# Kernel optimization log

Measured on AMD Instinct MI355X. Metric: run time of the kernel, lower is better.

## Reference

```python
import jax, jax.numpy as jnp
import numpy as np

SHIFT = 3
SHIFT2 = 1
POOL_K = 9
MAX_LEN = 16384
BATCH = 256


def _avg_pool1d(x, k, s):
    # x: [..., L] -> VALID average pool over last axis
    acc = jax.lax.reduce_window(x, 0.0, jax.lax.add,
                                (1,) * (x.ndim - 1) + (k,),
                                (1,) * (x.ndim - 1) + (s,), 'VALID')
    return acc / k


def _max_pool1d(x, k, s):
    return jax.lax.reduce_window(x, -jnp.inf, jax.lax.max,
                                 (1,) * (x.ndim - 1) + (k,),
                                 (1,) * (x.ndim - 1) + (s,), 'VALID')


def _upsample_nearest(x, size):
    # torch nn.Upsample(mode='nearest') to target length `size`
    m = x.shape[-1]
    idx = (jnp.arange(size) * m) // size
    return x[..., idx]


def setup_inputs() -> dict:
    key = jax.random.key(0)
    x = jax.random.normal(key, (BATCH, MAX_LEN), dtype=jnp.float32)
    return {"x": x}


def reference(x) -> jnp.ndarray:
    # First derivatives: fixed conv [[-1],[1]] over (rolled, original) row pairs
    # is exactly diff_d = x - roll(x, 2^d).  [B, shift, L]
    deriv1 = jnp.stack([x - jnp.roll(x, 1 << d, axis=-1) for d in range(SHIFT)], axis=1)
    # Second derivatives from the first diff channel (deriv1[:, 0]).
    d0 = deriv1[:, 0]
    deriv2 = jnp.stack([d0 - jnp.roll(d0, 1 << d, axis=-1) for d in range(SHIFT2)], axis=1)
    res = jnp.concatenate([deriv1, deriv2], axis=1)  # [B, shift+shift2, L]
    # Crop the wrapped-around prefix.
    off = max(1 << (SHIFT - 1), 1 << (SHIFT2 - 1))
    res = res[:, :, off:]
    # AvgPool1d(kernel=poolKernel, stride=1)
    res = _avg_pool1d(res, POOL_K, 1)  # [B, C, width]
    width = res.shape[-1]
    # MultiScale: four pool+upsample+residual branches, concat on channel dim.
    branches = [
        _upsample_nearest(_avg_pool1d(res, POOL_K, 1), width) + res,
        _upsample_nearest(_avg_pool1d(res, POOL_K, POOL_K), width) + res,
        _upsample_nearest(_max_pool1d(res, POOL_K, 1), width) + res,
        _upsample_nearest(_max_pool1d(res, POOL_K, POOL_K), width) + res,
    ]
    return jnp.concatenate(branches, axis=1)  # [B, 4*C, width]
```

## Files before the change

### kernel.cpp

```cpp
#include <hip/hip_runtime.h>

#define MAX_LEN 16384
#define RES_LEN 16372
#define P1_LEN  16364
#define P2_LEN  1819

__global__ __launch_bounds__(512, 2)
void derive_kernel(const float* __restrict__ x, float* __restrict__ out) {
    const int b = blockIdx.x >> 2;
    const int c = blockIdx.x & 3;
    const float* __restrict__ xr = x + (size_t)b * MAX_LEN;

    __shared__ float resS[RES_LEN + 4];
    __shared__ float a2S[P2_LEN + 1];
    __shared__ float m2S[P2_LEN + 1];

    const float inv9 = 1.0f / 9.0f;
    const int tid = threadIdx.x;

    if (c == 0) {
        for (int j = tid; j < RES_LEN; j += 512) {
            float W = xr[j + 12] - xr[j + 3];
            resS[j] = W * inv9;
        }
    } else if (c == 1) {
        for (int j = tid; j < RES_LEN; j += 512) {
            float W = (xr[j + 12] + xr[j + 11]) - (xr[j + 3] + xr[j + 2]);
            resS[j] = W * inv9;
        }
    } else if (c == 2) {
        for (int j = tid; j < RES_LEN; j += 512) {
            float W = (xr[j + 9] + xr[j + 10] + xr[j + 11] + xr[j + 12])
                    - (xr[j] + xr[j + 1] + xr[j + 2] + xr[j + 3]);
            resS[j] = W * inv9;
        }
    } else {
        for (int j = tid; j < RES_LEN; j += 512) {
            float W = (xr[j + 12] - xr[j + 11]) - (xr[j + 3] - xr[j + 2]);
            resS[j] = W * inv9;
        }
    }
    __syncthreads();

    for (int p = tid; p < P2_LEN; p += 512) {
        const int j0 = 9 * p;
        float v = resS[j0];
        float s = v, m = v;
        #pragma unroll
        for (int k = 1; k < 9; ++k) {
            float w = resS[j0 + k];
            s += w;
            m = fmaxf(m, w);
        }
        a2S[p] = s * inv9;
        m2S[p] = m;
    }
    __syncthreads();

    float* __restrict__ outBase = out + ((size_t)b * 16 + c) * RES_LEN;
    for (int i = tid; i < RES_LEN; i += 512) {
        const unsigned p1 = ((unsigned)i * 16364u) / 16372u;
        const unsigned p2 = ((unsigned)i * 1819u) / 16372u;

        float v = resS[p1];
        float s = v, m = v;
        #pragma unroll
        for (int k = 1; k < 9; ++k) {
            float w = resS[p1 + k];
            s += w;
            m = fmaxf(m, w);
        }
        const float r = resS[i];

        outBase[i]                    = s * inv9 + r;
        outBase[4 * RES_LEN + i]      = a2S[p2] + r;
        outBase[8 * RES_LEN + i]      = m + r;
        outBase[12 * RES_LEN + i]     = m2S[p2] + r;
    }
}

extern "C" void kernel_launch(void* const* d_in, const int* in_sizes, int n_in,
                              void* d_out, int out_size, void* d_ws, size_t ws_size,
                              hipStream_t stream) {
    const float* x = (const float*)d_in[0];
    float* out = (float*)d_out;
    derive_kernel<<<dim3(256 * 4), dim3(512), 0, stream>>>(x, out);
}
```

Before: 60.99 us.

## Vectorize loads and stores with float4 and sliding-window pooling per thread

Each thread now handles four consecutive outputs. Inputs are read as float4 and results written as float4, which replaces scalar global accesses. The stride-1 avg and max pools are computed from one 16-wide LDS window using a running sum and prefix/suffix max, with per-lane selection based on the upsample offset. Blocks are also remapped across batch rows, and launch bounds ask for more occupancy. Risks: the running-sum subtraction changes float rounding slightly, selection logic adds ALU work, and the higher occupancy target may spill registers.

```diff
diff --git a/kernel.cpp b/kernel.cpp
--- a/kernel.cpp
+++ b/kernel.cpp
@@ -2,80 +2,136 @@
 
 #define MAX_LEN 16384
 #define RES_LEN 16372
-#define P1_LEN  16364
 #define P2_LEN  1819
+#define NG      4093
 
-__global__ __launch_bounds__(512, 2)
+__global__ __launch_bounds__(512, 4)
 void derive_kernel(const float* __restrict__ x, float* __restrict__ out) {
-    const int b = blockIdx.x >> 2;
-    const int c = blockIdx.x & 3;
-    const float* __restrict__ xr = x + (size_t)b * MAX_LEN;
+    const int bid = blockIdx.x;
+    const int k_  = bid >> 3;
+    const int b   = ((bid & 7) << 5) | (k_ >> 2);
+    const int c   = k_ & 3;
 
-    __shared__ float resS[RES_LEN + 4];
-    __shared__ float a2S[P2_LEN + 1];
-    __shared__ float m2S[P2_LEN + 1];
+    const float*  __restrict__ xr  = x + (size_t)b * MAX_LEN;
+    const float4* __restrict__ xr4 = (const float4*)xr;
+
+    __shared__ float4 resS4[4096];
+    __shared__ float  a2S[P2_LEN + 1];
+    __shared__ float  m2S[P2_LEN + 1];
+    float* resS = (float*)resS4;
 
     const float inv9 = 1.0f / 9.0f;
     const int tid = threadIdx.x;
 
-    if (c == 0) {
-        for (int j = tid; j < RES_LEN; j += 512) {
-            float W = xr[j + 12] - xr[j + 3];
-            resS[j] = W * inv9;
+    for (int g = tid; g < NG; g += 512) {
+        float4 A = xr4[g], B4 = xr4[g + 1], C4 = xr4[g + 2], D4 = xr4[g + 3];
+        float xv[16];
+        xv[0]=A.x;  xv[1]=A.y;  xv[2]=A.z;  xv[3]=A.w;
+        xv[4]=B4.x; xv[5]=B4.y; xv[6]=B4.z; xv[7]=B4.w;
+        xv[8]=C4.x; xv[9]=C4.y; xv[10]=C4.z; xv[11]=C4.w;
+        xv[12]=D4.x; xv[13]=D4.y; xv[14]=D4.z; xv[15]=D4.w;
+        float rr[4];
+        if (c == 0) {
+            #pragma unroll
+            for (int j = 0; j < 4; ++j) rr[j] = (xv[j+12] - xv[j+3]) * inv9;
+        } else if (c == 1) {
+            #pragma unroll
+            for (int j = 0; j < 4; ++j) rr[j] = ((xv[j+12] + xv[j+11]) - (xv[j+3] + xv[j+2])) * inv9;
+        } else if (c == 2) {
+            #pragma unroll
+            for (int j = 0; j < 4; ++j) rr[j] = ((xv[j+9] + xv[j+10] + xv[j+11] + xv[j+12])
+                                               - (xv[j] + xv[j+1] + xv[j+2] + xv[j+3])) * inv9;
+        } else {
+            #pragma unroll
+            for (int j = 0; j < 4; ++j) rr[j] = ((xv[j+12] - xv[j+11]) - (xv[j+3] - xv[j+2])) * inv9;
         }
-    } else if (c == 1) {
-        for (int j = tid; j < RES_LEN; j += 512) {
-            float W = (xr[j + 12] + xr[j + 11]) - (xr[j + 3] + xr[j + 2]);
-            resS[j] = W * inv9;
-        }
-    } else if (c == 2) {
-        for (int j = tid; j < RES_LEN; j += 512) {
-            float W = (xr[j + 9] + xr[j + 10] + xr[j + 11] + xr[j + 12])
-                    - (xr[j] + xr[j + 1] + xr[j + 2] + xr[j + 3]);
-            resS[j] = W * inv9;
-        }
-    } else {
-        for (int j = tid; j < RES_LEN; j += 512) {
-            float W = (xr[j + 12] - xr[j + 11]) - (xr[j + 3] - xr[j + 2]);
-            resS[j] = W * inv9;
-        }
+        float4 rv; rv.x = rr[0]; rv.y = rr[1]; rv.z = rr[2]; rv.w = rr[3];
+        resS4[g] = rv;
     }
     __syncthreads();
 
     for (int p = tid; p < P2_LEN; p += 512) {
         const int j0 = 9 * p;
-        float v = resS[j0];
-        float s = v, m = v;
+        float s = resS[j0], m = resS[j0];
         #pragma unroll
-        for (int k = 1; k < 9; ++k) {
-            float w = resS[j0 + k];
-            s += w;
-            m = fmaxf(m, w);
-        }
-        a2S[p] = s * inv9;
-        m2S[p] = m;
+        for (int t = 1; t < 9; ++t) { float v = resS[j0 + t]; s += v; m = fmaxf(m, v); }
+        a2S[p] = s * inv9; m2S[p] = m;
     }
     __syncthreads();
 
-    float* __restrict__ outBase = out + ((size_t)b * 16 + c) * RES_LEN;
-    for (int i = tid; i < RES_LEN; i += 512) {
-        const unsigned p1 = ((unsigned)i * 16364u) / 16372u;
-        const unsigned p2 = ((unsigned)i * 1819u) / 16372u;
+    float* outBase = out + ((size_t)b * 16 + c) * RES_LEN;
+    float4* o0p = (float4*)(outBase);
+    float4* o1p = (float4*)(outBase + 4 * RES_LEN);
+    float4* o2p = (float4*)(outBase + 8 * RES_LEN);
+    float4* o3p = (float4*)(outBase + 12 * RES_LEN);
 
-        float v = resS[p1];
-        float s = v, m = v;
+    for (int g = tid; g < NG; g += 512) {
+        const unsigned i0 = 4u * (unsigned)g;
+        const unsigned p1_0 = (i0 * 16364u) / 16372u;
+        const unsigned p1_1 = ((i0 + 1u) * 16364u) / 16372u;
+        const unsigned p1_2 = ((i0 + 2u) * 16364u) / 16372u;
+        const unsigned p1_3 = ((i0 + 3u) * 16364u) / 16372u;
+        const unsigned p2_0 = (i0 * 1819u) / 16372u;
+        const unsigned p2_1 = ((i0 + 1u) * 1819u) / 16372u;
+        const unsigned p2_2 = ((i0 + 2u) * 1819u) / 16372u;
+        const unsigned p2_3 = ((i0 + 3u) * 1819u) / 16372u;
+        const unsigned q  = p1_0 >> 2;
+        const unsigned o0 = p1_0 & 3u;
+        const unsigned o1 = p1_1 - 4u * q;
+        const unsigned o2 = p1_2 - 4u * q;
+        const unsigned o3 = p1_3 - 4u * q;
+
+        float4 W0 = resS4[q], W1 = resS4[q + 1], W2 = resS4[q + 2], W3 = resS4[q + 3];
+        float w[16];
+        w[0]=W0.x;  w[1]=W0.y;  w[2]=W0.z;  w[3]=W0.w;
+        w[4]=W1.x;  w[5]=W1.y;  w[6]=W1.z;  w[7]=W1.w;
+        w[8]=W2.x;  w[9]=W2.y;  w[10]=W2.z; w[11]=W2.w;
+        w[12]=W3.x; w[13]=W3.y; w[14]=W3.z; w[15]=W3.w;
+
+        float s_[7];
+        s_[0] = ((((((((w[0] + w[1]) + w[2]) + w[3]) + w[4]) + w[5]) + w[6]) + w[7]) + w[8]);
         #pragma unroll
-        for (int k = 1; k < 9; ++k) {
-            float w = resS[p1 + k];
-            s += w;
-            m = fmaxf(m, w);
-        }
-        const float r = resS[i];
+        for (int e = 1; e < 7; ++e) s_[e] = s_[e - 1] - w[e - 1] + w[e + 8];
 
-        outBase[i]                    = s * inv9 + r;
-        outBase[4 * RES_LEN + i]      = a2S[p2] + r;
-        outBase[8 * RES_LEN + i]      = m + r;
-        outBase[12 * RES_LEN + i]     = m2S[p2] + r;
+        float suf[7];
+        suf[6] = fmaxf(fmaxf(w[6], w[7]), w[8]);
+        #pragma unroll
+        for (int t = 5; t >= 0; --t) suf[t] = fmaxf(w[t], suf[t + 1]);
+        float pre[15];
+        pre[8] = w[8];
+        #pragma unroll
+        for (int u = 9; u < 15; ++u) pre[u] = fmaxf(pre[u - 1], w[u]);
+        float m_[7];
+        #pragma unroll
+        for (int o = 0; o < 7; ++o) m_[o] = fmaxf(suf[o], pre[o + 8]);
+
+        float sum0 = s_[0], sum1 = s_[0], sum2 = s_[0], sum3 = s_[0];
+        float mx0  = m_[0], mx1  = m_[0], mx2  = m_[0], mx3  = m_[0];
+        #pragma unroll
+        for (int e = 1; e <= 3; ++e) { bool t_ = (o0 >= (unsigned)e); sum0 = t_ ? s_[e] : sum0; mx0 = t_ ? m_[e] : mx0; }
+        #pragma unroll
+        for (int e = 1; e <= 4; ++e) { bool t_ = (o1 >= (unsigned)e); sum1 = t_ ? s_[e] : sum1; mx1 = t_ ? m_[e] : mx1; }
+        #pragma unroll
+        for (int e = 1; e <= 5; ++e) { bool t_ = (o2 >= (unsigned)e); sum2 = t_ ? s_[e] : sum2; mx2 = t_ ? m_[e] : mx2; }
+        #pragma unroll
+        for (int e = 1; e <= 6; ++e) { bool t_ = (o3 >= (unsigned)e); sum3 = t_ ? s_[e] : sum3; mx3 = t_ ? m_[e] : mx3; }
+
+        const float4 R = resS4[g];
+
+        const float a2l = a2S[p2_0], a2h = a2S[p2_3];
+        const float m2l = m2S[p2_0], m2h = m2S[p2_3];
+        const float a2_1 = (p2_1 != p2_0) ? a2h : a2l;
+        const float a2_2 = (p2_2 != p2_0) ? a2h : a2l;
+        const float m2_1 = (p2_1 != p2_0) ? m2h : m2l;
+        const float m2_2 = (p2_2 != p2_0) ? m2h : m2l;
+
+        float4 v0, v1, v2, v3;
+        v0.x = sum0 * inv9 + R.x; v0.y = sum1 * inv9 + R.y; v0.z = sum2 * inv9 + R.z; v0.w = sum3 * inv9 + R.w;
+        v1.x = a2l + R.x;         v1.y = a2_1 + R.y;        v1.z = a2_2 + R.z;        v1.w = a2h + R.w;
+        v2.x = mx0 + R.x;         v2.y = mx1 + R.y;         v2.z = mx2 + R.z;         v2.w = mx3 + R.w;
+        v3.x = m2l + R.x;         v3.y = m2_1 + R.y;        v3.z = m2_2 + R.z;        v3.w = m2h + R.w;
+
+        o0p[g] = v0; o1p[g] = v1; o2p[g] = v2; o3p[g] = v3;
     }
 }
 
```

New measurement: 62.07 us. About the same (+1.8%).
